# Kernel tuning notes

Measured on AMD Instinct MI355X. Metric: run time of the kernel, lower is better.

The kernel has to match this reference:

```python
import jax, jax.numpy as jnp
import numpy as np

D_MODEL, N_LEVELS, N_HEADS, N_POINTS = 256, 4, 8, 4
HEAD_DIM = D_MODEL // N_HEADS
SPATIAL = np.array([[128, 128], [64, 64], [32, 32], [16, 16]], dtype=np.int64)
STARTS = np.concatenate([[0], np.cumsum(SPATIAL[:, 0] * SPATIAL[:, 1])[:-1]]).astype(np.int64)
N_TOK = int((SPATIAL[:, 0] * SPATIAL[:, 1]).sum())  # 21760
B, NQ = 2, 8192


def setup_inputs() -> dict:
    key = jax.random.key(0)
    ks = jax.random.split(key, 12)
    s = 1.0 / np.sqrt(D_MODEL)
    return {
        "query": jax.random.normal(ks[0], (B, NQ, D_MODEL), jnp.float32),
        "reference_points": jax.random.uniform(ks[1], (B, NQ, N_LEVELS, 2), jnp.float32),
        "input_flatten": jax.random.normal(ks[2], (B, N_TOK, D_MODEL), jnp.float32),
        "input_spatial_shapes": jnp.asarray(SPATIAL),
        "input_level_start_index": jnp.asarray(STARTS),
        "Wq": jax.random.normal(ks[3], (D_MODEL, D_MODEL), jnp.float32) * s,
        "bq": jnp.zeros((D_MODEL,), jnp.float32),
        "Wv": jax.random.normal(ks[4], (D_MODEL, D_MODEL), jnp.float32) * s,
        "bv": jnp.zeros((D_MODEL,), jnp.float32),
        "Wa": jax.random.normal(ks[5], (D_MODEL, N_HEADS * N_LEVELS * N_POINTS), jnp.float32) * s,
        "ba": jnp.zeros((N_HEADS * N_LEVELS * N_POINTS,), jnp.float32),
        "sampling_loc": jax.random.uniform(ks[6], (N_HEADS, N_LEVELS, N_POINTS, 2), jnp.float32, -0.1, 0.1),
        "Wo": jax.random.normal(ks[7], (D_MODEL, D_MODEL), jnp.float32) * s,
        "bo": jnp.zeros((D_MODEL,), jnp.float32),
    }


def _bilinear_sample(v_flat, grid, Hl, Wl):
    # v_flat: [B, H, Hl*Wl, Dh]; grid: [B, Nq, H, P, 2] in [-1, 1]
    b, nq, h, p, _ = grid.shape
    gx, gy = grid[..., 0], grid[..., 1]
    # align_corners=False pixel coordinates
    ix = ((gx + 1.0) * Wl - 1.0) * 0.5
    iy = ((gy + 1.0) * Hl - 1.0) * 0.5
    x0f, y0f = jnp.floor(ix), jnp.floor(iy)
    x0, y0 = x0f.astype(jnp.int32), y0f.astype(jnp.int32)
    x1, y1 = x0 + 1, y0 + 1
    wx1, wy1 = ix - x0f, iy - y0f
    wx0, wy0 = 1.0 - wx1, 1.0 - wy1

    def t(a):  # [B,Nq,H,P] -> [B,H,Nq*P]
        return a.transpose(0, 2, 1, 3).reshape(b, h, nq * p)

    def corner(yi, xi, w):
        valid = (xi >= 0) & (xi < Wl) & (yi >= 0) & (yi < Hl)
        idx = jnp.clip(yi, 0, Hl - 1) * Wl + jnp.clip(xi, 0, Wl - 1)
        g = jnp.take_along_axis(v_flat, t(idx)[..., None], axis=2)  # [B,H,Nq*P,Dh]
        return g * t(w * valid.astype(w.dtype))[..., None]

    out = (corner(y0, x0, wy0 * wx0) + corner(y0, x1, wy0 * wx1)
           + corner(y1, x0, wy1 * wx0) + corner(y1, x1, wy1 * wx1))
    return out.reshape(b, h, nq, p, -1)  # [B,H,Nq,P,Dh]


def reference(query, reference_points, input_flatten, input_spatial_shapes,
              input_level_start_index, Wq, bq, Wv, bv, Wa, ba, sampling_loc, Wo, bo):
    b, nq, c = query.shape
    h, L, p, _ = sampling_loc.shape
    dh = c // h
    q = query @ Wq + bq                                   # [B,Nq,C]
    attn = (q @ Wa + ba).reshape(b, nq, h, L, p)
    attn = jax.nn.softmax(attn, axis=-1)                  # softmax over points per level
    v = (input_flatten @ Wv + bv).reshape(b, -1, h, dh)   # [B,N,H,Dh]
    loc = reference_points[:, :, None, :, None, :] + sampling_loc[None, None]  # [B,Nq,H,L,P,2]
    grid = 2.0 * loc - 1.0
    shapes = np.asarray(input_spatial_shapes)
    starts = np.asarray(input_level_start_index)
    samples = []
    for lvl in range(L):
        Hl, Wl = int(shapes[lvl, 0]), int(shapes[lvl, 1])
        s0 = int(starts[lvl])
        vl = v[:, s0:s0 + Hl * Wl].transpose(0, 2, 1, 3)  # [B,H,Hl*Wl,Dh]
        samples.append(_bilinear_sample(vl, grid[:, :, :, lvl], Hl, Wl))
    samples = jnp.stack(samples, axis=3)                  # [B,H,Nq,L,P,Dh]
    out = jnp.einsum('bhnlpd,bnhlp->bnhd', samples, attn).reshape(b, nq, c)
    return out @ Wo + bo
```

## Files before the change

### kernel.cpp

```cpp
#include <hip/hip_runtime.h>
#include <hip/hip_bf16.h>

#define BATCH 2
#define NQ 8192
#define DM 256
#define NH 8
#define NL 4
#define NP 4
#define DH 32
#define NTOK 21760

typedef __attribute__((ext_vector_type(4))) float f32x4;
typedef __attribute__((ext_vector_type(8))) short s16x8;

static __device__ __forceinline__ unsigned short f2bu(float x) {
    __hip_bfloat16 h = __float2bfloat16(x);
    return __builtin_bit_cast(unsigned short, h);
}

__global__ void prep_kernel(const float* __restrict__ Wq, const float* __restrict__ Wa,
                            const float* __restrict__ bq, const float* __restrict__ ba,
                            const float* __restrict__ Wv, const float* __restrict__ Wo,
                            float* __restrict__ Wqa, float* __restrict__ bqa,
                            unsigned short* __restrict__ WvT, unsigned short* __restrict__ WoT) {
    const int i = blockIdx.x;
    const int j = threadIdx.x;
    WvT[j * 256 + i] = f2bu(Wv[i * 256 + j]);
    WoT[j * 256 + i] = f2bu(Wo[i * 256 + j]);
    if (j < 128) {
        float acc = 0.f;
        for (int k = 0; k < 256; ++k) acc += Wq[i * 256 + k] * Wa[k * 128 + j];
        Wqa[i * 128 + j] = acc;
        if (i == 0) {
            float bacc = ba[j];
            for (int k = 0; k < 256; ++k) bacc += bq[k] * Wa[k * 128 + j];
            bqa[j] = bacc;
        }
    }
}

template <bool AFP32, bool BF16OUT>
__global__ __launch_bounds__(256) void gemm_mfma(
    const void* __restrict__ Av, const unsigned short* __restrict__ Bt,
    const float* __restrict__ bias, void* __restrict__ Cv,
    int M, int N, int K) {
    __shared__ __align__(16) char As[128 * 64 * 2];
    __shared__ __align__(16) char Bs[128 * 64 * 2];
    const int tid = threadIdx.x;
    const int lane = tid & 63;
    const int wave = tid >> 6;
    const int wr = wave >> 1, wc = wave & 1;
    const int bm = blockIdx.y * 128;
    const int bn = blockIdx.x * 128;

    f32x4 acc[4][4] = {};

    const int srow = tid >> 3;
    const int skc = (tid & 7) * 8;

    for (int k0 = 0; k0 < K; k0 += 64) {
#pragma unroll
        for (int r = 0; r < 4; ++r) {
            const int row = srow + r * 32;
            const int byte = (row * 128 + skc * 2) ^ ((row & 7) << 4);
            s16x8 av;
            if (AFP32) {
                const float* Af = (const float*)Av + (size_t)(bm + row) * K + k0 + skc;
                const float4 f0 = *(const float4*)(Af);
                const float4 f1 = *(const float4*)(Af + 4);
                av[0] = (short)f2bu(f0.x); av[1] = (short)f2bu(f0.y);
                av[2] = (short)f2bu(f0.z); av[3] = (short)f2bu(f0.w);
                av[4] = (short)f2bu(f1.x); av[5] = (short)f2bu(f1.y);
                av[6] = (short)f2bu(f1.z); av[7] = (short)f2bu(f1.w);
            } else {
                av = *(const s16x8*)((const unsigned short*)Av + (size_t)(bm + row) * K + k0 + skc);
            }
            *(s16x8*)(As + byte) = av;
            const s16x8 bv = *(const s16x8*)(Bt + (size_t)(bn + row) * K + k0 + skc);
            *(s16x8*)(Bs + byte) = bv;
        }
        __syncthreads();
#pragma unroll
        for (int f = 0; f < 2; ++f) {
            s16x8 a[4], b[4];
#pragma unroll
            for (int i = 0; i < 4; ++i) {
                const int arow = wr * 64 + i * 16 + (lane & 15);
                const int abyte = (arow * 128 + f * 64 + (lane >> 4) * 16) ^ ((arow & 7) << 4);
                a[i] = *(const s16x8*)(As + abyte);
                const int brow = wc * 64 + i * 16 + (lane & 15);
                const int bbyte = (brow * 128 + f * 64 + (lane >> 4) * 16) ^ ((brow & 7) << 4);
                b[i] = *(const s16x8*)(Bs + bbyte);
            }
#pragma unroll
            for (int i = 0; i < 4; ++i)
#pragma unroll
                for (int j = 0; j < 4; ++j)
                    acc[i][j] = __builtin_amdgcn_mfma_f32_16x16x32_bf16(a[i], b[j], acc[i][j], 0, 0, 0);
        }
        __syncthreads();
    }

#pragma unroll
    for (int i = 0; i < 4; ++i) {
        const int row0 = bm + wr * 64 + i * 16 + (lane >> 4) * 4;
#pragma unroll
        for (int j = 0; j < 4; ++j) {
            const int col = bn + wc * 64 + j * 16 + (lane & 15);
            const float bsv = bias[col];
#pragma unroll
            for (int q = 0; q < 4; ++q) {
                const float val = acc[i][j][q] + bsv;
                if (BF16OUT)
                    ((unsigned short*)Cv)[(size_t)(row0 + q) * N + col] = f2bu(val);
                else
                    ((float*)Cv)[(size_t)(row0 + q) * N + col] = val;
            }
        }
    }
}

#define AROWS 8
__global__ void attn_kernel(const float* __restrict__ query, const float* __restrict__ Wqa,
                            const float* __restrict__ bqa, float* __restrict__ attn) {
    const int row0 = blockIdx.x * AROWS;
    const int tid = threadIdx.x;
    __shared__ float qs[AROWS][256];
    for (int i = tid; i < AROWS * 256; i += 128)
        qs[i >> 8][i & 255] = query[(size_t)row0 * 256 + i];
    __syncthreads();
    float acc[AROWS];
    const float b0 = bqa[tid];
#pragma unroll
    for (int r = 0; r < AROWS; ++r) acc[r] = b0;
    for (int k = 0; k < 256; ++k) {
        const float w = Wqa[k * 128 + tid];
#pragma unroll
        for (int r = 0; r < AROWS; ++r) acc[r] += qs[r][k] * w;
    }
    __shared__ float lg[AROWS][128];
#pragma unroll
    for (int r = 0; r < AROWS; ++r) lg[r][tid] = acc[r];
    __syncthreads();
    const int g = tid & ~3;
#pragma unroll
    for (int r = 0; r < AROWS; ++r) {
        const float m = fmaxf(fmaxf(lg[r][g], lg[r][g + 1]), fmaxf(lg[r][g + 2], lg[r][g + 3]));
        const float e0 = __expf(lg[r][g] - m), e1 = __expf(lg[r][g + 1] - m);
        const float e2 = __expf(lg[r][g + 2] - m), e3 = __expf(lg[r][g + 3] - m);
        attn[((size_t)(row0 + r)) * 128 + tid] = __expf(acc[r] - m) / (e0 + e1 + e2 + e3);
    }
}

__global__ __launch_bounds__(256) void sample_kernel(
    const float* __restrict__ refp, const float* __restrict__ sloc,
    const unsigned int* __restrict__ v,
    const float* __restrict__ attn,
    unsigned int* __restrict__ samp) {
    const int tid = threadIdx.x;
    const int q0 = blockIdx.x * 2;
    const int qi = tid >> 7;
    const int sub = tid & 127;
    const int h = sub >> 4;
    const int dp = sub & 15;
    const int bq = q0 + qi;
    const int b = bq >> 13;

    __shared__ float sl[NH][NL][NP][2];
    __shared__ float rp[2][NL * 2];
    __shared__ float at[2][128];

    {
        const int c = tid & 1, p = (tid >> 1) & 3, l = (tid >> 3) & 3, hh = tid >> 5;
        const float scale = (float)(128 >> l);
        sl[hh][l][p][c] = sloc[((hh * NL + l) * NP + p) * 2 + c] * scale - 0.5f;
    }
    if (tid < 16) rp[tid >> 3][tid & 7] = refp[(size_t)q0 * 8 + tid];
    at[qi][sub] = attn[(size_t)bq * 128 + sub];
    __syncthreads();

    const int vq = b * (NTOK * 128) + h * 16 + dp;
    float acc0 = 0.f, acc1 = 0.f;
    const int WLs[4] = {128, 64, 32, 16};
    const int SSs[4] = {0, 16384, 20480, 21504};
#pragma unroll
    for (int l = 0; l < NL; ++l) {
        const int Wl = WLs[l];
        const float fW = (float)Wl;
        const int base = vq + SSs[l] * 128;
        const float rx = rp[qi][l * 2], ry = rp[qi][l * 2 + 1];
#pragma unroll
        for (int p = 0; p < NP; ++p) {
            const float ix = fmaf(rx, fW, sl[h][l][p][0]);
            const float iy = fmaf(ry, fW, sl[h][l][p][1]);
            const float xf = floorf(ix), yf = floorf(iy);
            const int x0 = (int)xf, y0 = (int)yf;
            const int x1 = x0 + 1, y1 = y0 + 1;
            float wx1 = ix - xf, wy1 = iy - yf;
            float wx0 = 1.f - wx1, wy0 = 1.f - wy1;
            const float a = at[qi][h * 16 + l * 4 + p];
            wx0 = ((unsigned)x0 < (unsigned)Wl) ? wx0 : 0.f;
            wx1 = ((unsigned)x1 < (unsigned)Wl) ? wx1 : 0.f;
            wy0 = ((unsigned)y0 < (unsigned)Wl) ? wy0 * a : 0.f;
            wy1 = ((unsigned)y1 < (unsigned)Wl) ? wy1 * a : 0.f;
            const int x0c = min(max(x0, 0), Wl - 1);
            const int x1c = min(max(x1, 0), Wl - 1);
            const int y0c = min(max(y0, 0), Wl - 1);
            const int y1c = min(max(y1, 0), Wl - 1);
            const int r0 = y0c * Wl, r1 = y1c * Wl;
            const unsigned int u00 = v[base + (r0 + x0c) * 128];
            const unsigned int u01 = v[base + (r0 + x1c) * 128];
            const unsigned int u10 = v[base + (r1 + x0c) * 128];
            const unsigned int u11 = v[base + (r1 + x1c) * 128];
            const float w00 = wy0 * wx0, w01 = wy0 * wx1;
            const float w10 = wy1 * wx0, w11 = wy1 * wx1;
            acc0 = fmaf(__uint_as_float(u00 << 16), w00, acc0);
            acc1 = fmaf(__uint_as_float(u00 & 0xffff0000u), w00, acc1);
            acc0 = fmaf(__uint_as_float(u01 << 16), w01, acc0);
            acc1 = fmaf(__uint_as_float(u01 & 0xffff0000u), w01, acc1);
            acc0 = fmaf(__uint_as_float(u10 << 16), w10, acc0);
            acc1 = fmaf(__uint_as_float(u10 & 0xffff0000u), w10, acc1);
            acc0 = fmaf(__uint_as_float(u11 << 16), w11, acc0);
            acc1 = fmaf(__uint_as_float(u11 & 0xffff0000u), w11, acc1);
        }
    }
    const unsigned int us = (unsigned int)f2bu(acc0) | ((unsigned int)f2bu(acc1) << 16);
    samp[(size_t)bq * 128 + h * 16 + dp] = us;
}

extern "C" void kernel_launch(void* const* d_in, const int* in_sizes, int n_in,
                              void* d_out, int out_size, void* d_ws, size_t ws_size,
                              hipStream_t stream) {
    const float* query  = (const float*)d_in[0];
    const float* refp   = (const float*)d_in[1];
    const float* inflat = (const float*)d_in[2];
    const float* Wq = (const float*)d_in[5];
    const float* bq = (const float*)d_in[6];
    const float* Wv = (const float*)d_in[7];
    const float* bv = (const float*)d_in[8];
    const float* Wa = (const float*)d_in[9];
    const float* ba = (const float*)d_in[10];
    const float* sloc = (const float*)d_in[11];
    const float* Wo = (const float*)d_in[12];
    const float* bo = (const float*)d_in[13];
    float* out = (float*)d_out;

    char* ws = (char*)d_ws;
    float* Wqa = (float*)(ws + 0);
    float* bqa = (float*)(ws + (128u << 10));
    unsigned short* WvT = (unsigned short*)(ws + (192u << 10));
    unsigned short* WoT = (unsigned short*)(ws + (320u << 10));
    unsigned int* vbuf = (unsigned int*)(ws + (1u << 20));
    float* attn = (float*)(ws + (24u << 20));
    unsigned int* samp = (unsigned int*)(ws + (32u << 20));

    prep_kernel<<<256, 256, 0, stream>>>(Wq, Wa, bq, ba, Wv, Wo, Wqa, bqa, WvT, WoT);
    gemm_mfma<true, true><<<dim3(2, 340), 256, 0, stream>>>(inflat, WvT, bv, vbuf, BATCH * NTOK, 256, 256);
    attn_kernel<<<(BATCH * NQ) / AROWS, 128, 0, stream>>>(query, Wqa, bqa, attn);
    sample_kernel<<<BATCH * NQ / 2, 256, 0, stream>>>(refp, sloc, (const unsigned int*)vbuf, attn, samp);
    gemm_mfma<false, false><<<dim3(2, 128), 256, 0, stream>>>(samp, WoT, bo, out, BATCH * NQ, 256, 256);
}
```

Measured before the change: 241.9 us.

## Move attention logits to MFMA GEMM, fuse softmax into sampling, prefetch GEMM tiles

The scalar attention-logit kernel is replaced by the templated bf16 MFMA GEMM using a folded, transposed Wq·Wa weight, and the per-level softmax now runs inside the sampling kernel through wave shuffles. The sampling kernel is restructured in two phases: sample metadata (corner indices and weights) is computed once per point into shared memory, then each thread gathers 4 channels with vector loads. The GEMM gains register double-buffered prefetch of the next K tile, configurable tile shapes and a fixed K. Weight prep is split into a tiled shared-memory transpose and a separate Wqa kernel. Logits now pass through bf16 inputs, which costs some precision.

```diff
diff --git a/kernel.cpp b/kernel.cpp
--- a/kernel.cpp
+++ b/kernel.cpp
@@ -3,11 +3,6 @@
 
 #define BATCH 2
 #define NQ 8192
-#define DM 256
-#define NH 8
-#define NL 4
-#define NP 4
-#define DH 32
 #define NTOK 21760
 
 typedef __attribute__((ext_vector_type(4))) float f32x4;
@@ -17,101 +12,153 @@
     __hip_bfloat16 h = __float2bfloat16(x);
     return __builtin_bit_cast(unsigned short, h);
 }
-
-__global__ void prep_kernel(const float* __restrict__ Wq, const float* __restrict__ Wa,
-                            const float* __restrict__ bq, const float* __restrict__ ba,
-                            const float* __restrict__ Wv, const float* __restrict__ Wo,
-                            float* __restrict__ Wqa, float* __restrict__ bqa,
-                            unsigned short* __restrict__ WvT, unsigned short* __restrict__ WoT) {
+static __device__ __forceinline__ float blo(unsigned int u) { return __uint_as_float(u << 16); }
+static __device__ __forceinline__ float bhi(unsigned int u) { return __uint_as_float(u & 0xffff0000u); }
+
+__global__ void wqa_kernel(const float* __restrict__ Wq, const float* __restrict__ Wa,
+                           const float* __restrict__ bq, const float* __restrict__ ba,
+                           unsigned short* __restrict__ WqaT, float* __restrict__ bqa) {
     const int i = blockIdx.x;
     const int j = threadIdx.x;
-    WvT[j * 256 + i] = f2bu(Wv[i * 256 + j]);
-    WoT[j * 256 + i] = f2bu(Wo[i * 256 + j]);
-    if (j < 128) {
-        float acc = 0.f;
-        for (int k = 0; k < 256; ++k) acc += Wq[i * 256 + k] * Wa[k * 128 + j];
-        Wqa[i * 128 + j] = acc;
-        if (i == 0) {
-            float bacc = ba[j];
-            for (int k = 0; k < 256; ++k) bacc += bq[k] * Wa[k * 128 + j];
-            bqa[j] = bacc;
-        }
-    }
-}
-
-template <bool AFP32, bool BF16OUT>
+    float acc = 0.f;
+#pragma unroll 8
+    for (int k = 0; k < 256; ++k) acc += Wq[i * 256 + k] * Wa[k * 128 + j];
+    WqaT[j * 256 + i] = f2bu(acc);
+    if (i == 0) {
+        float b = ba[j];
+#pragma unroll 8
+        for (int k = 0; k < 256; ++k) b += bq[k] * Wa[k * 128 + j];
+        bqa[j] = b;
+    }
+}
+
+__global__ __launch_bounds__(256) void transpose_kernel(const float* __restrict__ Wv, const float* __restrict__ Wo,
+                                                        unsigned short* __restrict__ WvT, unsigned short* __restrict__ WoT) {
+    __shared__ float t[32][33];
+    const int bid = blockIdx.x;
+    const int mat = bid >> 6;
+    const int tile = bid & 63;
+    const int i0 = (tile >> 3) * 32, j0 = (tile & 7) * 32;
+    const float* src = mat ? Wo : Wv;
+    unsigned short* dst = mat ? WoT : WvT;
+    const int tx = threadIdx.x & 31, ty = threadIdx.x >> 5;
+#pragma unroll
+    for (int r = 0; r < 4; ++r)
+        t[ty + 8 * r][tx] = src[(i0 + ty + 8 * r) * 256 + j0 + tx];
+    __syncthreads();
+#pragma unroll
+    for (int r = 0; r < 4; ++r)
+        dst[(j0 + ty + 8 * r) * 256 + i0 + tx] = f2bu(t[tx][ty + 8 * r]);
+}
+
+template <int BM, int BN, int WRN, int WCN, bool AFP32, bool BF16OUT>
 __global__ __launch_bounds__(256) void gemm_mfma(
     const void* __restrict__ Av, const unsigned short* __restrict__ Bt,
-    const float* __restrict__ bias, void* __restrict__ Cv,
-    int M, int N, int K) {
-    __shared__ __align__(16) char As[128 * 64 * 2];
-    __shared__ __align__(16) char Bs[128 * 64 * 2];
+    const float* __restrict__ bias, void* __restrict__ Cv, int N) {
+    constexpr int K = 256, NT = 4;
+    constexpr int IM = BM / (WRN * 16);
+    constexpr int JN = BN / (WCN * 16);
+    constexpr int RA = BM / 32;
+    constexpr int RB = BN / 32;
+    __shared__ __align__(16) char As[BM * 128];
+    __shared__ __align__(16) char Bs[BN * 128];
     const int tid = threadIdx.x;
     const int lane = tid & 63;
     const int wave = tid >> 6;
-    const int wr = wave >> 1, wc = wave & 1;
-    const int bm = blockIdx.y * 128;
-    const int bn = blockIdx.x * 128;
-
-    f32x4 acc[4][4] = {};
-
+    const int wr = wave / WCN, wc = wave % WCN;
+    const int bm = blockIdx.y * BM, bn = blockIdx.x * BN;
     const int srow = tid >> 3;
     const int skc = (tid & 7) * 8;
 
-    for (int k0 = 0; k0 < K; k0 += 64) {
-#pragma unroll
-        for (int r = 0; r < 4; ++r) {
+    f32x4 acc[IM][JN] = {};
+    float4 af0[2][RA], af1[2][RA];
+    s16x8 ab[2][RA], bb[2][RB];
+
+    auto loadT = [&](int t, int buf) {
+        const int k0 = t * 64;
+#pragma unroll
+        for (int r = 0; r < RA; ++r) {
+            const int row = bm + srow + r * 32;
+            if constexpr (AFP32) {
+                const float* Af = (const float*)Av + (size_t)row * K + k0 + skc;
+                af0[buf][r] = *(const float4*)Af;
+                af1[buf][r] = *(const float4*)(Af + 4);
+            } else {
+                ab[buf][r] = *(const s16x8*)((const unsigned short*)Av + (size_t)row * K + k0 + skc);
+            }
+        }
+#pragma unroll
+        for (int r = 0; r < RB; ++r) {
+            const int row = bn + srow + r * 32;
+            bb[buf][r] = *(const s16x8*)(Bt + (size_t)row * K + k0 + skc);
+        }
+    };
+    auto writeT = [&](int buf) {
+#pragma unroll
+        for (int r = 0; r < RA; ++r) {
             const int row = srow + r * 32;
             const int byte = (row * 128 + skc * 2) ^ ((row & 7) << 4);
             s16x8 av;
-            if (AFP32) {
-                const float* Af = (const float*)Av + (size_t)(bm + row) * K + k0 + skc;
-                const float4 f0 = *(const float4*)(Af);
-                const float4 f1 = *(const float4*)(Af + 4);
+            if constexpr (AFP32) {
+                const float4 f0 = af0[buf][r], f1 = af1[buf][r];
                 av[0] = (short)f2bu(f0.x); av[1] = (short)f2bu(f0.y);
                 av[2] = (short)f2bu(f0.z); av[3] = (short)f2bu(f0.w);
                 av[4] = (short)f2bu(f1.x); av[5] = (short)f2bu(f1.y);
                 av[6] = (short)f2bu(f1.z); av[7] = (short)f2bu(f1.w);
             } else {
-                av = *(const s16x8*)((const unsigned short*)Av + (size_t)(bm + row) * K + k0 + skc);
+                av = ab[buf][r];
             }
             *(s16x8*)(As + byte) = av;
-            const s16x8 bv = *(const s16x8*)(Bt + (size_t)(bn + row) * K + k0 + skc);
-            *(s16x8*)(Bs + byte) = bv;
-        }
+        }
+#pragma unroll
+        for (int r = 0; r < RB; ++r) {
+            const int row = srow + r * 32;
+            const int byte = (row * 128 + skc * 2) ^ ((row & 7) << 4);
+            *(s16x8*)(Bs + byte) = bb[buf][r];
+        }
+    };
+
+    loadT(0, 0);
+#pragma unroll
+    for (int t = 0; t < NT; ++t) {
+        if (t) __syncthreads();
+        writeT(t & 1);
+        if (t + 1 < NT) loadT(t + 1, (t + 1) & 1);
         __syncthreads();
 #pragma unroll
         for (int f = 0; f < 2; ++f) {
-            s16x8 a[4], b[4];
-#pragma unroll
-            for (int i = 0; i < 4; ++i) {
-                const int arow = wr * 64 + i * 16 + (lane & 15);
+            s16x8 a[IM], b[JN];
+#pragma unroll
+            for (int i = 0; i < IM; ++i) {
+                const int arow = wr * (IM * 16) + i * 16 + (lane & 15);
                 const int abyte = (arow * 128 + f * 64 + (lane >> 4) * 16) ^ ((arow & 7) << 4);
                 a[i] = *(const s16x8*)(As + abyte);
-                const int brow = wc * 64 + i * 16 + (lane & 15);
+            }
+#pragma unroll
+            for (int j = 0; j < JN; ++j) {
+                const int brow = wc * (JN * 16) + j * 16 + (lane & 15);
                 const int bbyte = (brow * 128 + f * 64 + (lane >> 4) * 16) ^ ((brow & 7) << 4);
-                b[i] = *(const s16x8*)(Bs + bbyte);
-            }
-#pragma unroll
-            for (int i = 0; i < 4; ++i)
-#pragma unroll
-                for (int j = 0; j < 4; ++j)
+                b[j] = *(const s16x8*)(Bs + bbyte);
+            }
+#pragma unroll
+            for (int i = 0; i < IM; ++i)
+#pragma unroll
+                for (int j = 0; j < JN; ++j)
                     acc[i][j] = __builtin_amdgcn_mfma_f32_16x16x32_bf16(a[i], b[j], acc[i][j], 0, 0, 0);
         }
-        __syncthreads();
-    }
-
-#pragma unroll
-    for (int i = 0; i < 4; ++i) {
-        const int row0 = bm + wr * 64 + i * 16 + (lane >> 4) * 4;
-#pragma unroll
-        for (int j = 0; j < 4; ++j) {
-            const int col = bn + wc * 64 + j * 16 + (lane & 15);
+    }
+
+#pragma unroll
+    for (int i = 0; i < IM; ++i) {
+        const int row0 = bm + wr * (IM * 16) + i * 16 + (lane >> 4) * 4;
+#pragma unroll
+        for (int j = 0; j < JN; ++j) {
+            const int col = bn + wc * (JN * 16) + j * 16 + (lane & 15);
             const float bsv = bias[col];
 #pragma unroll
             for (int q = 0; q < 4; ++q) {
                 const float val = acc[i][j][q] + bsv;
-                if (BF16OUT)
+                if constexpr (BF16OUT)
                     ((unsigned short*)Cv)[(size_t)(row0 + q) * N + col] = f2bu(val);
                 else
                     ((float*)Cv)[(size_t)(row0 + q) * N + col] = val;
@@ -120,112 +167,98 @@
     }
 }
 
-#define AROWS 8
-__global__ void attn_kernel(const float* __restrict__ query, const float* __restrict__ Wqa,
-                            const float* __restrict__ bqa, float* __restrict__ attn) {
-    const int row0 = blockIdx.x * AROWS;
-    const int tid = threadIdx.x;
-    __shared__ float qs[AROWS][256];
-    for (int i = tid; i < AROWS * 256; i += 128)
-        qs[i >> 8][i & 255] = query[(size_t)row0 * 256 + i];
-    __syncthreads();
-    float acc[AROWS];
-    const float b0 = bqa[tid];
-#pragma unroll
-    for (int r = 0; r < AROWS; ++r) acc[r] = b0;
-    for (int k = 0; k < 256; ++k) {
-        const float w = Wqa[k * 128 + tid];
-#pragma unroll
-        for (int r = 0; r < AROWS; ++r) acc[r] += qs[r][k] * w;
-    }
-    __shared__ float lg[AROWS][128];
-#pragma unroll
-    for (int r = 0; r < AROWS; ++r) lg[r][tid] = acc[r];
-    __syncthreads();
-    const int g = tid & ~3;
-#pragma unroll
-    for (int r = 0; r < AROWS; ++r) {
-        const float m = fmaxf(fmaxf(lg[r][g], lg[r][g + 1]), fmaxf(lg[r][g + 2], lg[r][g + 3]));
-        const float e0 = __expf(lg[r][g] - m), e1 = __expf(lg[r][g + 1] - m);
-        const float e2 = __expf(lg[r][g + 2] - m), e3 = __expf(lg[r][g + 3] - m);
-        attn[((size_t)(row0 + r)) * 128 + tid] = __expf(acc[r] - m) / (e0 + e1 + e2 + e3);
-    }
-}
-
 __global__ __launch_bounds__(256) void sample_kernel(
     const float* __restrict__ refp, const float* __restrict__ sloc,
     const unsigned int* __restrict__ v,
-    const float* __restrict__ attn,
+    const float* __restrict__ logits,
     unsigned int* __restrict__ samp) {
     const int tid = threadIdx.x;
-    const int q0 = blockIdx.x * 2;
-    const int qi = tid >> 7;
-    const int sub = tid & 127;
-    const int h = sub >> 4;
-    const int dp = sub & 15;
+    const int q0 = blockIdx.x * 4;
+    __shared__ int4 metaI[512];
+    __shared__ float4 metaW[512];
+    __shared__ float slc[256];
+    __shared__ float lgs[512];
+    __shared__ float rps[32];
+
+    {
+        const int l = (tid >> 3) & 3;
+        slc[tid] = sloc[tid] * (float)(128 >> l) - 0.5f;
+    }
+    lgs[tid] = logits[(size_t)q0 * 128 + tid];
+    lgs[tid + 256] = logits[(size_t)q0 * 128 + tid + 256];
+    if (tid < 32) rps[tid] = refp[(size_t)q0 * 8 + tid];
+    __syncthreads();
+
+#pragma unroll
+    for (int ss = 0; ss < 2; ++ss) {
+        const int h = tid & 7;
+        const int p = (tid >> 3) & 3;
+        const int l = (tid >> 5) & 3;
+        const int qi = (tid >> 7) + ss * 2;
+        const int lp = l * 4 + p;
+        const int bq = q0 + qi;
+        const int b = bq >> 13;
+        const int Wl = 128 >> l;
+        const float lg = lgs[qi * 128 + h * 16 + lp];
+        float m = fmaxf(lg, __shfl_xor(lg, 8));
+        m = fmaxf(m, __shfl_xor(m, 16));
+        const float e = __expf(lg - m);
+        float sum = e + __shfl_xor(e, 8);
+        sum += __shfl_xor(sum, 16);
+        const float a = e / sum;
+        const float fW = (float)Wl;
+        const float ix = fmaf(rps[qi * 8 + l * 2 + 0], fW, slc[h * 32 + l * 8 + p * 2 + 0]);
+        const float iy = fmaf(rps[qi * 8 + l * 2 + 1], fW, slc[h * 32 + l * 8 + p * 2 + 1]);
+        const float xf = floorf(ix), yf = floorf(iy);
+        const int x0 = (int)xf, y0 = (int)yf;
+        const int x1 = x0 + 1, y1 = y0 + 1;
+        float wx1 = ix - xf, wy1 = iy - yf;
+        float wx0 = 1.f - wx1, wy0 = 1.f - wy1;
+        wx0 = ((unsigned)x0 < (unsigned)Wl) ? wx0 : 0.f;
+        wx1 = ((unsigned)x1 < (unsigned)Wl) ? wx1 : 0.f;
+        wy0 = ((unsigned)y0 < (unsigned)Wl) ? wy0 * a : 0.f;
+        wy1 = ((unsigned)y1 < (unsigned)Wl) ? wy1 * a : 0.f;
+        const int x0c = min(max(x0, 0), Wl - 1);
+        const int x1c = min(max(x1, 0), Wl - 1);
+        const int y0c = min(max(y0, 0), Wl - 1);
+        const int y1c = min(max(y1, 0), Wl - 1);
+        const int SS = (65536 - (65536 >> (2 * l))) / 3;
+        const int base = b * (NTOK * 128) + SS * 128 + h * 16;
+        const int r0 = y0c * Wl, r1 = y1c * Wl;
+        const int s = lp * 32 + qi * 8 + h;
+        metaI[s] = make_int4(base + (r0 + x0c) * 128, base + (r0 + x1c) * 128,
+                             base + (r1 + x0c) * 128, base + (r1 + x1c) * 128);
+        metaW[s] = make_float4(wy0 * wx0, wy0 * wx1, wy1 * wx0, wy1 * wx1);
+    }
+    __syncthreads();
+
+    const int qi = tid >> 6, h = (tid >> 3) & 7, c = tid & 7;
+    const unsigned int* vp = v + c * 2;
+    float a0 = 0.f, a1 = 0.f, a2 = 0.f, a3 = 0.f;
+#pragma unroll
+    for (int lp = 0; lp < 16; ++lp) {
+        const int s = lp * 32 + qi * 8 + h;
+        const int4 I = metaI[s];
+        const float4 W = metaW[s];
+        uint2 u;
+        u = *(const uint2*)(vp + I.x);
+        a0 = fmaf(blo(u.x), W.x, a0); a1 = fmaf(bhi(u.x), W.x, a1);
+        a2 = fmaf(blo(u.y), W.x, a2); a3 = fmaf(bhi(u.y), W.x, a3);
+        u = *(const uint2*)(vp + I.y);
+        a0 = fmaf(blo(u.x), W.y, a0); a1 = fmaf(bhi(u.x), W.y, a1);
+        a2 = fmaf(blo(u.y), W.y, a2); a3 = fmaf(bhi(u.y), W.y, a3);
+        u = *(const uint2*)(vp + I.z);
+        a0 = fmaf(blo(u.x), W.z, a0); a1 = fmaf(bhi(u.x), W.z, a1);
+        a2 = fmaf(blo(u.y), W.z, a2); a3 = fmaf(bhi(u.y), W.z, a3);
+        u = *(const uint2*)(vp + I.w);
+        a0 = fmaf(blo(u.x), W.w, a0); a1 = fmaf(bhi(u.x), W.w, a1);
+        a2 = fmaf(blo(u.y), W.w, a2); a3 = fmaf(bhi(u.y), W.w, a3);
+    }
     const int bq = q0 + qi;
-    const int b = bq >> 13;
-
-    __shared__ float sl[NH][NL][NP][2];
-    __shared__ float rp[2][NL * 2];
-    __shared__ float at[2][128];
-
-    {
-        const int c = tid & 1, p = (tid >> 1) & 3, l = (tid >> 3) & 3, hh = tid >> 5;
-        const float scale = (float)(128 >> l);
-        sl[hh][l][p][c] = sloc[((hh * NL + l) * NP + p) * 2 + c] * scale - 0.5f;
-    }
-    if (tid < 16) rp[tid >> 3][tid & 7] = refp[(size_t)q0 * 8 + tid];
-    at[qi][sub] = attn[(size_t)bq * 128 + sub];
-    __syncthreads();
-
-    const int vq = b * (NTOK * 128) + h * 16 + dp;
-    float acc0 = 0.f, acc1 = 0.f;
-    const int WLs[4] = {128, 64, 32, 16};
-    const int SSs[4] = {0, 16384, 20480, 21504};
-#pragma unroll
-    for (int l = 0; l < NL; ++l) {
-        const int Wl = WLs[l];
-        const float fW = (float)Wl;
-        const int base = vq + SSs[l] * 128;
-        const float rx = rp[qi][l * 2], ry = rp[qi][l * 2 + 1];
-#pragma unroll
-        for (int p = 0; p < NP; ++p) {
-            const float ix = fmaf(rx, fW, sl[h][l][p][0]);
-            const float iy = fmaf(ry, fW, sl[h][l][p][1]);
-            const float xf = floorf(ix), yf = floorf(iy);
-            const int x0 = (int)xf, y0 = (int)yf;
-            const int x1 = x0 + 1, y1 = y0 + 1;
-            float wx1 = ix - xf, wy1 = iy - yf;
-            float wx0 = 1.f - wx1, wy0 = 1.f - wy1;
-            const float a = at[qi][h * 16 + l * 4 + p];
-            wx0 = ((unsigned)x0 < (unsigned)Wl) ? wx0 : 0.f;
-            wx1 = ((unsigned)x1 < (unsigned)Wl) ? wx1 : 0.f;
-            wy0 = ((unsigned)y0 < (unsigned)Wl) ? wy0 * a : 0.f;
-            wy1 = ((unsigned)y1 < (unsigned)Wl) ? wy1 * a : 0.f;
-            const int x0c = min(max(x0, 0), Wl - 1);
-            const int x1c = min(max(x1, 0), Wl - 1);
-            const int y0c = min(max(y0, 0), Wl - 1);
-            const int y1c = min(max(y1, 0), Wl - 1);
-            const int r0 = y0c * Wl, r1 = y1c * Wl;
-            const unsigned int u00 = v[base + (r0 + x0c) * 128];
-            const unsigned int u01 = v[base + (r0 + x1c) * 128];
-            const unsigned int u10 = v[base + (r1 + x0c) * 128];
-            const unsigned int u11 = v[base + (r1 + x1c) * 128];
-            const float w00 = wy0 * wx0, w01 = wy0 * wx1;
-            const float w10 = wy1 * wx0, w11 = wy1 * wx1;
-            acc0 = fmaf(__uint_as_float(u00 << 16), w00, acc0);
-            acc1 = fmaf(__uint_as_float(u00 & 0xffff0000u), w00, acc1);
-            acc0 = fmaf(__uint_as_float(u01 << 16), w01, acc0);
-            acc1 = fmaf(__uint_as_float(u01 & 0xffff0000u), w01, acc1);
-            acc0 = fmaf(__uint_as_float(u10 << 16), w10, acc0);
-            acc1 = fmaf(__uint_as_float(u10 & 0xffff0000u), w10, acc1);
-            acc0 = fmaf(__uint_as_float(u11 << 16), w11, acc0);
-            acc1 = fmaf(__uint_as_float(u11 & 0xffff0000u), w11, acc1);
-        }
-    }
-    const unsigned int us = (unsigned int)f2bu(acc0) | ((unsigned int)f2bu(acc1) << 16);
-    samp[(size_t)bq * 128 + h * 16 + dp] = us;
+    uint2 o;
+    o.x = (unsigned)f2bu(a0) | ((unsigned)f2bu(a1) << 16);
+    o.y = (unsigned)f2bu(a2) | ((unsigned)f2bu(a3) << 16);
+    *(uint2*)(samp + (size_t)bq * 128 + h * 16 + c * 2) = o;
 }
 
 extern "C" void kernel_launch(void* const* d_in, const int* in_sizes, int n_in,
@@ -246,17 +279,18 @@
     float* out = (float*)d_out;
 
     char* ws = (char*)d_ws;
-    float* Wqa = (float*)(ws + 0);
-    float* bqa = (float*)(ws + (128u << 10));
-    unsigned short* WvT = (unsigned short*)(ws + (192u << 10));
-    unsigned short* WoT = (unsigned short*)(ws + (320u << 10));
+    unsigned short* WqaT = (unsigned short*)(ws + 0);
+    float* bqa = (float*)(ws + (64u << 10));
+    unsigned short* WvT = (unsigned short*)(ws + (128u << 10));
+    unsigned short* WoT = (unsigned short*)(ws + (256u << 10));
     unsigned int* vbuf = (unsigned int*)(ws + (1u << 20));
-    float* attn = (float*)(ws + (24u << 20));
+    float* logits = (float*)(ws + (24u << 20));
     unsigned int* samp = (unsigned int*)(ws + (32u << 20));
 
-    prep_kernel<<<256, 256, 0, stream>>>(Wq, Wa, bq, ba, Wv, Wo, Wqa, bqa, WvT, WoT);
-    gemm_mfma<true, true><<<dim3(2, 340), 256, 0, stream>>>(inflat, WvT, bv, vbuf, BATCH * NTOK, 256, 256);
-    attn_kernel<<<(BATCH * NQ) / AROWS, 128, 0, stream>>>(query, Wqa, bqa, attn);
-    sample_kernel<<<BATCH * NQ / 2, 256, 0, stream>>>(refp, sloc, (const unsigned int*)vbuf, attn, samp);
-    gemm_mfma<false, false><<<dim3(2, 128), 256, 0, stream>>>(samp, WoT, bo, out, BATCH * NQ, 256, 256);
-}
+    wqa_kernel<<<256, 128, 0, stream>>>(Wq, Wa, bq, ba, WqaT, bqa);
+    transpose_kernel<<<128, 256, 0, stream>>>(Wv, Wo, WvT, WoT);
+    gemm_mfma<128, 128, 2, 2, true, true><<<dim3(2, 340), 256, 0, stream>>>(inflat, WvT, bv, vbuf, 256);
+    gemm_mfma<64, 64, 2, 2, true, false><<<dim3(2, 256), 256, 0, stream>>>(query, WqaT, bqa, logits, 128);
+    sample_kernel<<<BATCH * NQ / 4, 256, 0, stream>>>(refp, sloc, (const unsigned int*)vbuf, logits, samp);
+    gemm_mfma<64, 128, 1, 4, false, false><<<dim3(2, 256), 256, 0, stream>>>(samp, WoT, bo, out, 256);
+}
```

After: 206.8 us. -14.5%, faster.
